# Kernel tuning notes

Hardware: AMD Instinct MI355X
Metric: run time of the kernel (lower is better)

The kernel has to match this reference:

```python
import jax, jax.numpy as jnp
import numpy as np

B, N, F_DIM, G_DIM, E_CAT, N_HEAD = 8, 1024, 128, 64, 2, 4
N_EDGES = 16384
L0 = 256          # NodeEmbedding hidden layer (layers=[256,128] -> last replaced by feature_size)
ALPHA = 0.5       # cfg.alpha
EPS = 1e-5        # BatchNorm eps
SLOPE = 0.01      # leaky_relu default negative slope


def _glorot(k, shape):
    stdv = float(np.sqrt(6.0 / (shape[-2] + shape[-1])))
    return jax.random.uniform(k, shape, jnp.float32, -stdv, stdv)


def setup_inputs() -> dict:
    key = jax.random.key(0)
    ks = jax.random.split(key, 8)
    X = jax.random.normal(ks[0], (B, N, F_DIM), dtype=jnp.float32)
    A = jax.random.randint(ks[1], (B, E_CAT, 2, N_EDGES), 0, N, dtype=jnp.int32)
    Ws = _glorot(ks[2], (E_CAT, N_HEAD * F_DIM, G_DIM))
    Wq = _glorot(ks[3], (E_CAT, N_HEAD * F_DIM, 1))
    Wv = _glorot(ks[4], (E_CAT, N_HEAD * F_DIM, 1))
    W_emb1 = _glorot(ks[5], (F_DIM, N_HEAD * E_CAT * G_DIM))   # Embedding1, bias=False
    W_lin0 = _glorot(ks[6], (L0, F_DIM))                        # NodeEmbedding linear0
    W_lin1 = _glorot(ks[7], (F_DIM, L0))                        # NodeEmbedding linear1
    return {"A": A, "X": X, "Ws": Ws, "Wq": Wq, "Wv": Wv,
            "W_emb1": W_emb1, "W_lin0": W_lin0, "W_lin1": W_lin1, "mini_batch": 1}


def _bn(x):
    # BatchNorm1d in training mode, affine = identity (weight=1, bias=0)
    mu = jnp.mean(x, axis=0)
    var = jnp.var(x, axis=0)  # biased variance, as torch uses for normalization
    return (x - mu) * jax.lax.rsqrt(var + EPS)


def _build_adj(A):
    # torch.sparse_coo_tensor(...).to_dense() sums duplicate edges
    adj = jnp.zeros((B, E_CAT, N, N), jnp.float32)
    b_idx = jnp.arange(B)[:, None, None]
    e_idx = jnp.arange(E_CAT)[None, :, None]
    return adj.at[b_idx, e_idx, A[:, :, 0], A[:, :, 1]].add(1.0)


def reference(A, X, Ws, Wq, Wv, W_emb1, W_lin0, W_lin1, mini_batch):
    Ws_r = Ws.reshape(E_CAT, N_HEAD, F_DIM, G_DIM)
    Wq_r = Wq.reshape(E_CAT, N_HEAD, F_DIM)   # last dim of Wq param is 1
    Wv_r = Wv.reshape(E_CAT, N_HEAD, F_DIM)

    Wh = jnp.einsum('bnf,ehfg->behng', X, Ws_r)   # [B,E,H,N,G]
    q = jnp.einsum('bnf,ehf->behn', X, Wq_r)      # [B,E,H,N]
    v = jnp.einsum('bnf,ehf->behn', X, Wv_r)

    adj = _build_adj(A)                            # [B,E,N,N]
    # e = (Wq @ Wv.T) * E, then leaky_relu and row softmax (dim=1 on [N,N] = last axis)
    scores = q[:, :, :, :, None] * v[:, :, :, None, :] * adj[:, :, None]
    scores = jnp.where(scores >= 0, scores, SLOPE * scores)
    a = jax.nn.softmax(scores, axis=-1)
    H = jnp.einsum('behnm,behmg->behng', a, Wh)    # [B,E,H,N,G]

    # concat over heads: [B,N, head-major (E*G)]
    H = H.transpose(0, 3, 2, 1, 4).reshape(B * N, N_HEAD * E_CAT * G_DIM)
    H = jax.nn.relu(H @ W_emb1.T)
    Xf = X.reshape(B * N, F_DIM)
    H = _bn((1.0 - ALPHA) * H + ALPHA * Xf)

    # NodeEmbedding: Linear -> BN -> ELU -> Linear
    Z = jax.nn.elu(_bn(H @ W_lin0.T))
    Z = Z @ W_lin1.T
    Z = _bn(H + Z)
    return Z.reshape(B, N, F_DIM)
```

## Files before the change

### kernel.cpp

```cpp
#include <hip/hip_runtime.h>
#include <hip/hip_bf16.h>

#define B_    8
#define N_    1024
#define F_    128
#define G_    64
#define EC    2
#define NHD   4
#define NE    16384
#define L0_   256
#define ALPHA_ 0.5f
#define EPS_   1e-5f
#define SLOPE_ 0.01f
#define ROWS  (B_*N_)
#define C1    (NHD*EC*G_)

typedef __attribute__((ext_vector_type(8))) short s8bf;
typedef __attribute__((ext_vector_type(4))) float f32x4;

__device__ __forceinline__ float ldv(const float* p, size_t i) { return p[i]; }
__device__ __forceinline__ float ldv(const __hip_bfloat16* p, size_t i) {
  unsigned short u = *(const unsigned short*)&p[i];
  return __uint_as_float((unsigned)u << 16);
}
__device__ __forceinline__ unsigned short f2b(float f) {
  unsigned u = __float_as_uint(f);
  u = (u + 0x7FFFu + ((u >> 16) & 1u)) >> 16;
  return (unsigned short)u;
}
__device__ __forceinline__ float b2f(unsigned short u) {
  return __uint_as_float((unsigned)u << 16);
}

__device__ __forceinline__ float wmaxf(float v) {
#pragma unroll
  for (int o = 32; o; o >>= 1) v = fmaxf(v, __shfl_xor(v, o, 64));
  return v;
}
__device__ __forceinline__ float wsumf(float v) {
#pragma unroll
  for (int o = 32; o; o >>= 1) v += __shfl_xor(v, o, 64);
  return v;
}

__global__ void k_detect(const unsigned short* Xu, int* flag) {
  int idx = blockIdx.x * 256 + threadIdx.x;
  unsigned short u = Xu[idx];
  if ((u & 0x7F80u) == 0x7F80u) atomicOr(flag, 1);
}

__device__ __forceinline__ unsigned short cvt_at(const void* p, size_t i, int isf) {
  return isf ? f2b(((const float*)p)[i]) : ((const unsigned short*)p)[i];
}
__global__ void k_cvtw(const void* X, const void* Ws, const void* We1, const void* Wl1,
                       unsigned short* Xb, unsigned short* Wsb, unsigned short* We1b,
                       unsigned short* Wl1b, const int* flag) {
  int isf = *flag;
  int bid = blockIdx.x, t = threadIdx.x;
  if (bid < 4096) {
    int i = bid * 256 + t; Xb[i] = cvt_at(X, i, isf);
  } else if (bid < 4352) {
    int i = (bid - 4096) * 256 + t; We1b[i] = cvt_at(We1, i, isf);
  } else if (bid < 4480) {
    int i = (bid - 4352) * 256 + t; Wl1b[i] = cvt_at(Wl1, i, isf);
  } else {
    int i = (bid - 4480) * 256 + t;
    int eh = i >> 13, rem = i & 8191;
    int g = rem >> 7, f = rem & 127;
    Wsb[eh * 8192 + g * 128 + f] = cvt_at(Ws, (size_t)eh * 8192 + f * 64 + g, isf);
  }
}

template <typename T>
__device__ __forceinline__ void proj_qv_body(const T* X, const T* Wq, const T* Wv,
                                             float* q, float* v) {
  int tid = threadIdx.x, lane = tid & 63, w = tid >> 6;
  int r = blockIdx.x * 4 + w;
  int n = r & (N_ - 1); int beh = r >> 10; int be = beh >> 2, h = beh & 3;
  int b = be >> 1, e = be & 1;
  const T* xr = X + ((size_t)(b * N_ + n)) * F_;
  const T* wq = Wq + (e * NHD + h) * F_;
  const T* wv = Wv + (e * NHD + h) * F_;
  float x0 = ldv(xr, lane), x1 = ldv(xr, lane + 64);
  float aq = x0 * ldv(wq, lane) + x1 * ldv(wq, lane + 64);
  float av = x0 * ldv(wv, lane) + x1 * ldv(wv, lane + 64);
  aq = wsumf(aq); av = wsumf(av);
  if (lane == 0) { q[r] = aq; v[r] = av; }
}
__global__ void k_proj_qv(const void* X, const void* Wq, const void* Wv,
                          float* q, float* v, const int* flag) {
  if (*flag) proj_qv_body<float>((const float*)X, (const float*)Wq, (const float*)Wv, q, v);
  else       proj_qv_body<__hip_bfloat16>((const __hip_bfloat16*)X, (const __hip_bfloat16*)Wq,
                                          (const __hip_bfloat16*)Wv, q, v);
}

template <int K>
__device__ __forceinline__ void mfma_core(const unsigned short* __restrict__ Ab,
                                          const unsigned short* __restrict__ Wb,
                                          int r0, int c0, f32x4* acc) {
  int lane = threadIdx.x & 63; int q = lane >> 4, c15 = lane & 15;
  constexpr int RS = K / 8;
  const s8bf* ap = (const s8bf*)Ab + (size_t)(r0 + c15) * RS + q;
  const s8bf* bp = (const s8bf*)Wb + (size_t)(c0 + c15) * RS + q;
#pragma unroll
  for (int ks = 0; ks < K / 32; ++ks) {
    s8bf a  = ap[ks * 4];
    s8bf b0 = bp[ks * 4];
    s8bf b1 = bp[16 * RS + ks * 4];
    s8bf b2 = bp[32 * RS + ks * 4];
    s8bf b3 = bp[48 * RS + ks * 4];
    acc[0] = __builtin_amdgcn_mfma_f32_16x16x32_bf16(a, b0, acc[0], 0, 0, 0);
    acc[1] = __builtin_amdgcn_mfma_f32_16x16x32_bf16(a, b1, acc[1], 0, 0, 0);
    acc[2] = __builtin_amdgcn_mfma_f32_16x16x32_bf16(a, b2, acc[2], 0, 0, 0);
    acc[3] = __builtin_amdgcn_mfma_f32_16x16x32_bf16(a, b3, acc[3], 0, 0, 0);
  }
}

__global__ __launch_bounds__(64) void k_whm(const unsigned short* Xb,
                                            const unsigned short* Wsb,
                                            float* Wh, float* S) {
  int r0 = blockIdx.x * 16; int eh = blockIdx.y;
  f32x4 acc[4] = {{0,0,0,0},{0,0,0,0},{0,0,0,0},{0,0,0,0}};
  mfma_core<128>(Xb, Wsb + eh * 8192, r0, 0, acc);
  int lane = threadIdx.x, q = lane >> 4, c15 = lane & 15;
  int b = r0 >> 10; int beh = b * 8 + eh;
  float* WhB = Wh + ((size_t)beh * N_ + (r0 & (N_ - 1))) * G_;
#pragma unroll
  for (int nc = 0; nc < 4; ++nc) {
    float s = 0.f;
#pragma unroll
    for (int i = 0; i < 4; ++i) {
      float o = acc[nc][i];
      WhB[(size_t)(q * 4 + i) * G_ + nc * 16 + c15] = o;
      s += o;
    }
    s += __shfl_xor(s, 16, 64); s += __shfl_xor(s, 32, 64);
    if (lane < 16) atomicAdd(&S[(size_t)beh * G_ + nc * 16 + lane], s);
  }
}

__global__ void k_scatter2(const int* A, int* fill, int* colbuf) {
  int idx = blockIdx.x * 256 + threadIdx.x;
  int be = idx >> 14, i = idx & (NE - 1);
  int row = A[(size_t)(be * 2) * NE + i];
  int col = A[(size_t)(be * 2 + 1) * NE + i];
  int p = atomicAdd(&fill[be * N_ + row], 1);
  if (p < 64) colbuf[((size_t)(be * N_ + row)) * 64 + p] = col;
}

__global__ __launch_bounds__(256) void k_attn2(const float* q, const float* v, const float* Wh,
                                               const float* S, const int* fill,
                                               const int* colbuf, unsigned short* Hcatb) {
  __shared__ int s_col[64];
  __shared__ int s_cnt[64];
  __shared__ int s_ld;
  __shared__ float s_w[4][64];
  int tid = threadIdx.x, lane = tid & 63, h = tid >> 6;
  int be = blockIdx.x >> 10, n = blockIdx.x & (N_ - 1);
  int b = be >> 1, e = be & 1;
  if (h == 0) {
    s_col[lane] = 0;
    int L = fill[be * N_ + n];
    int Lc = (L > 64) ? 64 : L;
    int myc = (lane < Lc) ? colbuf[((size_t)(be * N_ + n)) * 64 + lane] : -1;
    int cct = 0, firstk = 64;
    for (int k = 0; k < Lc; ++k) {
      int ck = __shfl(myc, k, 64);
      if (myc >= 0 && ck == myc) { cct++; if (k < firstk) firstk = k; }
    }
    bool act = (lane < Lc) && (firstk == lane);
    unsigned long long mask = __ballot(act);
    int pos = __popcll(mask & ((1ull << lane) - 1ull));
    if (act) { s_col[pos] = myc; s_cnt[pos] = cct; }
    if (lane == 0) s_ld = __popcll(mask);
  }
  __syncthreads();
  int Ld = s_ld;
  int beh = (be << 2) | h;
  float qn = q[beh * N_ + n];
  float sc = -1e30f;
  if (lane < Ld) {
    float t = qn * v[beh * N_ + s_col[lane]] * (float)s_cnt[lane];
    sc = (t >= 0.f) ? t : SLOPE_ * t;
  }
  float M = fmaxf(0.f, wmaxf(sc));
  float Ej = (lane < Ld) ? expf(sc - M) : 0.f;
  float sumE = wsumf(Ej);
  float em = expf(-M);
  float Z = (float)(N_ - Ld) * em + sumE;
  s_w[h][lane] = (lane < Ld) ? (Ej - em) / Z : 0.f;
  int eg = lane >> 4, g4 = (lane & 15) << 2;
  float4 accv = make_float4(0.f, 0.f, 0.f, 0.f);
  if (eg == 0) {
    float4 s4 = *(const float4*)&S[(size_t)beh * G_ + g4];
    float sca = em / Z;
    accv.x = sca * s4.x; accv.y = sca * s4.y; accv.z = sca * s4.z; accv.w = sca * s4.w;
  }
  const float* WhB = Wh + (size_t)beh * N_ * G_;
  for (int k0 = 0; k0 < Ld; k0 += 4) {
    int kk = k0 + eg;
    float wk = s_w[h][kk];
    int ck = s_col[kk];
    float4 x = *(const float4*)&WhB[(size_t)ck * G_ + g4];
    accv.x += wk * x.x; accv.y += wk * x.y; accv.z += wk * x.z; accv.w += wk * x.w;
  }
  accv.x += __shfl_xor(accv.x, 16, 64); accv.y += __shfl_xor(accv.y, 16, 64);
  accv.z += __shfl_xor(accv.z, 16, 64); accv.w += __shfl_xor(accv.w, 16, 64);
  accv.x += __shfl_xor(accv.x, 32, 64); accv.y += __shfl_xor(accv.y, 32, 64);
  accv.z += __shfl_xor(accv.z, 32, 64); accv.w += __shfl_xor(accv.w, 32, 64);
  if (lane < 16) {
    ushort4 o;
    o.x = f2b(accv.x); o.y = f2b(accv.y); o.z = f2b(accv.z); o.w = f2b(accv.w);
    *(ushort4*)&Hcatb[((size_t)(b * N_ + n)) * C1 + h * (EC * G_) + e * G_ + g4] = o;
  }
}

template <typename TX>
__device__ __forceinline__ void mm1_ep(f32x4* acc, const TX* X, float* T4,
                                       unsigned short* T4b, float* sum1, float* ssq1,
                                       int r0, int c0) {
  int lane = threadIdx.x, q = lane >> 4, c15 = lane & 15;
#pragma unroll
  for (int nc = 0; nc < 4; ++nc) {
    int cc = c0 + nc * 16 + c15;
    float s = 0.f, s2 = 0.f;
#pragma unroll
    for (int i = 0; i < 4; ++i) {
      int rr = r0 + q * 4 + i;
      float o = fmaxf(acc[nc][i], 0.f);
      o = 0.5f * o + 0.5f * ldv(X, (size_t)rr * F_ + cc);
      T4[(size_t)rr * F_ + cc] = o;
      T4b[(size_t)rr * F_ + cc] = f2b(o);
      s += o; s2 += o * o;
    }
    s += __shfl_xor(s, 16, 64); s += __shfl_xor(s, 32, 64);
    s2 += __shfl_xor(s2, 16, 64); s2 += __shfl_xor(s2, 32, 64);
    if (lane < 16) {
      atomicAdd(&sum1[c0 + nc * 16 + lane], s);
      atomicAdd(&ssq1[c0 + nc * 16 + lane], s2);
    }
  }
}
__global__ __launch_bounds__(64) void k_mm1m(const unsigned short* Hcatb,
                                             const unsigned short* We1b, const void* X,
                                             float* T4, unsigned short* T4b,
                                             float* sum1, float* ssq1, const int* flag) {
  int r0 = blockIdx.x * 16, c0 = blockIdx.y * 64;
  f32x4 acc[4] = {{0,0,0,0},{0,0,0,0},{0,0,0,0},{0,0,0,0}};
  mfma_core<512>(Hcatb, We1b, r0, c0, acc);
  if (*flag) mm1_ep<float>(acc, (const float*)X, T4, T4b, sum1, ssq1, r0, c0);
  else       mm1_ep<__hip_bfloat16>(acc, (const __hip_bfloat16*)X, T4, T4b, sum1, ssq1, r0, c0);
}

__global__ void k_fold0(const void* Wl0, const float* sum1, const float* ssq1,
                        unsigned short* W0p, float* bias0, const int* flag) {
  __shared__ float red[2];
  int c = blockIdx.x, k = threadIdx.x;
  float mean = sum1[k] * (1.f / ROWS);
  float var = ssq1[k] * (1.f / ROWS) - mean * mean;
  float rs = rsqrtf(var + EPS_);
  float w = (*flag) ? ((const float*)Wl0)[(size_t)c * F_ + k]
                    : b2f(((const unsigned short*)Wl0)[(size_t)c * F_ + k]);
  unsigned short wb = f2b(w * rs);
  W0p[(size_t)c * F_ + k] = wb;
  float part = mean * b2f(wb);
  part = wsumf(part);
  if ((threadIdx.x & 63) == 0) red[threadIdx.x >> 6] = part;
  __syncthreads();
  if (threadIdx.x == 0) bias0[c] = red[0] + red[1];
}

__global__ __launch_bounds__(64) void k_lin0m(const unsigned short* T4b,
                                              const unsigned short* W0p, const float* bias0,
                                              float* Z0, float* sum2, float* ssq2) {
  int r0 = blockIdx.x * 16, c0 = blockIdx.y * 64;
  f32x4 acc[4] = {{0,0,0,0},{0,0,0,0},{0,0,0,0},{0,0,0,0}};
  mfma_core<128>(T4b, W0p, r0, c0, acc);
  int lane = threadIdx.x, q = lane >> 4, c15 = lane & 15;
#pragma unroll
  for (int nc = 0; nc < 4; ++nc) {
    int cc = c0 + nc * 16 + c15;
    float bia = bias0[cc];
    float s = 0.f, s2 = 0.f;
#pragma unroll
    for (int i = 0; i < 4; ++i) {
      int rr = r0 + q * 4 + i;
      float o = acc[nc][i] - bia;
      Z0[(size_t)rr * L0_ + cc] = o;
      s += o; s2 += o * o;
    }
    s += __shfl_xor(s, 16, 64); s += __shfl_xor(s, 32, 64);
    s2 += __shfl_xor(s2, 16, 64); s2 += __shfl_xor(s2, 32, 64);
    if (lane < 16) {
      atomicAdd(&sum2[c0 + nc * 16 + lane], s);
      atomicAdd(&ssq2[c0 + nc * 16 + lane], s2);
    }
  }
}

__global__ void k_elu(const float* Z0, unsigned short* E, const float* sum2,
                      const float* ssq2) {
  int idx = blockIdx.x * 256 + threadIdx.x;
  int c = idx & (L0_ - 1);
  float mean = sum2[c] * (1.f / ROWS);
  float var = ssq2[c] * (1.f / ROWS) - mean * mean;
  float y = (Z0[idx] - mean) * rsqrtf(var + EPS_);
  y = (y > 0.f) ? y : (expf(y) - 1.f);
  E[idx] = f2b(y);
}

__global__ __launch_bounds__(64) void k_lin1m(const unsigned short* E,
                                              const unsigned short* Wl1b, const float* T4,
                                              const float* sum1, const float* ssq1,
                                              float* T6, float* sum3, float* ssq3) {
  int r0 = blockIdx.x * 16, c0 = blockIdx.y * 64;
  f32x4 acc[4] = {{0,0,0,0},{0,0,0,0},{0,0,0,0},{0,0,0,0}};
  mfma_core<256>(E, Wl1b, r0, c0, acc);
  int lane = threadIdx.x, q = lane >> 4, c15 = lane & 15;
#pragma unroll
  for (int nc = 0; nc < 4; ++nc) {
    int cc = c0 + nc * 16 + c15;
    float mean = sum1[cc] * (1.f / ROWS);
    float var = ssq1[cc] * (1.f / ROWS) - mean * mean;
    float rs = rsqrtf(var + EPS_);
    float s = 0.f, s2 = 0.f;
#pragma unroll
    for (int i = 0; i < 4; ++i) {
      int rr = r0 + q * 4 + i;
      float o = acc[nc][i] + (T4[(size_t)rr * F_ + cc] - mean) * rs;
      T6[(size_t)rr * F_ + cc] = o;
      s += o; s2 += o * o;
    }
    s += __shfl_xor(s, 16, 64); s += __shfl_xor(s, 32, 64);
    s2 += __shfl_xor(s2, 16, 64); s2 += __shfl_xor(s2, 32, 64);
    if (lane < 16) {
      atomicAdd(&sum3[c0 + nc * 16 + lane], s);
      atomicAdd(&ssq3[c0 + nc * 16 + lane], s2);
    }
  }
}

__global__ void k_norm_out(const float* in, void* out, const float* sum, const float* ssq,
                           const int* flag) {
  int idx = blockIdx.x * 256 + threadIdx.x; int c = idx & (F_ - 1);
  float mean = sum[c] * (1.f / ROWS);
  float var = ssq[c] * (1.f / ROWS) - mean * mean;
  float y = (in[idx] - mean) * rsqrtf(var + EPS_);
  if (*flag) ((float*)out)[idx] = y;
  else       ((__hip_bfloat16*)out)[idx] = __float2bfloat16(y);
}

extern "C" void kernel_launch(void* const* d_in, const int* in_sizes, int n_in,
                              void* d_out, int out_size, void* d_ws, size_t ws_size,
                              hipStream_t stream) {
  const int* A    = (const int*)d_in[0];
  const void* X   = d_in[1];
  const void* Ws  = d_in[2];
  const void* Wq  = d_in[3];
  const void* Wv  = d_in[4];
  const void* We1 = d_in[5];
  const void* Wl0 = d_in[6];
  const void* Wl1 = d_in[7];

  char* ws = (char*)d_ws;
  size_t off = 0;
  auto alloc = [&](size_t bytes) { size_t o = off; off += (bytes + 255) & ~(size_t)255; return o; };
  size_t o_fill   = alloc(16 * N_ * 4);
  size_t o_stats  = alloc(1024 * 4);
  size_t o_flag   = alloc(256);
  size_t o_S      = alloc((size_t)64 * G_ * 4);
  size_t zero_bytes = off;
  size_t o_colbuf = alloc((size_t)16 * N_ * 64 * 4);
  size_t o_q      = alloc((size_t)64 * N_ * 4);
  size_t o_v      = alloc((size_t)64 * N_ * 4);
  size_t o_Wh     = alloc((size_t)64 * N_ * G_ * 4);
  size_t o_Hcatb  = alloc((size_t)ROWS * C1 * 2);
  size_t o_T4     = alloc((size_t)ROWS * F_ * 4);
  size_t o_T4b    = alloc((size_t)ROWS * F_ * 2);
  size_t o_T6     = alloc((size_t)ROWS * F_ * 4);
  size_t o_Z0     = alloc((size_t)ROWS * L0_ * 4);
  size_t o_E      = alloc((size_t)ROWS * L0_ * 2);
  size_t o_Xb     = alloc((size_t)ROWS * F_ * 2);
  size_t o_Wsb    = alloc((size_t)8 * G_ * F_ * 2);
  size_t o_We1b   = alloc((size_t)F_ * C1 * 2);
  size_t o_Wl1b   = alloc((size_t)F_ * L0_ * 2);
  size_t o_W0p    = alloc((size_t)L0_ * F_ * 2);
  size_t o_bias0  = alloc(L0_ * 4);

  int*   fill   = (int*)(ws + o_fill);
  float* stats  = (float*)(ws + o_stats);
  int*   flag   = (int*)(ws + o_flag);
  float* S      = (float*)(ws + o_S);
  int*   colbuf = (int*)(ws + o_colbuf);
  float* q      = (float*)(ws + o_q);
  float* v      = (float*)(ws + o_v);
  float* Wh     = (float*)(ws + o_Wh);
  unsigned short* Hcatb = (unsigned short*)(ws + o_Hcatb);
  float* T4     = (float*)(ws + o_T4);
  unsigned short* T4b   = (unsigned short*)(ws + o_T4b);
  float* T6     = (float*)(ws + o_T6);
  float* Z0     = (float*)(ws + o_Z0);
  unsigned short* E     = (unsigned short*)(ws + o_E);
  unsigned short* Xb    = (unsigned short*)(ws + o_Xb);
  unsigned short* Wsb   = (unsigned short*)(ws + o_Wsb);
  unsigned short* We1b  = (unsigned short*)(ws + o_We1b);
  unsigned short* Wl1b  = (unsigned short*)(ws + o_Wl1b);
  unsigned short* W0p   = (unsigned short*)(ws + o_W0p);
  float* bias0  = (float*)(ws + o_bias0);
  float* sum1 = stats,       *ssq1 = stats + 128;
  float* sum2 = stats + 256, *ssq2 = stats + 512;
  float* sum3 = stats + 768, *ssq3 = stats + 896;

  hipMemsetAsync(ws, 0, zero_bytes, stream);

  k_detect<<<512, 256, 0, stream>>>((const unsigned short*)X, flag);
  k_cvtw<<<4736, 256, 0, stream>>>(X, Ws, We1, Wl1, Xb, Wsb, We1b, Wl1b, flag);

  k_proj_qv<<<(64 * N_) / 4, 256, 0, stream>>>(X, Wq, Wv, q, v, flag);
  k_whm<<<dim3(ROWS / 16, 8), 64, 0, stream>>>(Xb, Wsb, Wh, S);

  k_scatter2<<<(16 * NE) / 256, 256, 0, stream>>>(A, fill, colbuf);
  k_attn2<<<16 * N_, 256, 0, stream>>>(q, v, Wh, S, fill, colbuf, Hcatb);

  k_mm1m<<<dim3(ROWS / 16, 2), 64, 0, stream>>>(Hcatb, We1b, X, T4, T4b, sum1, ssq1, flag);
  k_fold0<<<L0_, 128, 0, stream>>>(Wl0, sum1, ssq1, W0p, bias0, flag);
  k_lin0m<<<dim3(ROWS / 16, 4), 64, 0, stream>>>(T4b, W0p, bias0, Z0, sum2, ssq2);
  k_elu<<<(ROWS * L0_) / 256, 256, 0, stream>>>(Z0, E, sum2, ssq2);
  k_lin1m<<<dim3(ROWS / 16, 2), 64, 0, stream>>>(E, Wl1b, T4, sum1, ssq1, T6, sum3, ssq3);
  k_norm_out<<<(ROWS * F_) / 256, 256, 0, stream>>>(T6, d_out, sum3, ssq3, flag);

  (void)in_sizes; (void)n_in; (void)out_size; (void)ws_size;
}
```

Before: 247.3 us.

## Fuse BatchNorm/ELU into GEMM A-loads, store Wh in bf16, restructure attention per wave

Removes the k_fold0 and k_elu kernels. The BatchNorm normalisation (and the ELU for the second linear) is now applied inside the MFMA A-operand load, reading fp32 activations and converting to bf16 on the fly. Wh is stored as bf16 to halve gather traffic in attention. The attention kernel now handles one node per wave across all four heads, using shuffles instead of shared memory and syncthreads. The trade-off is extra ALU work and fp32 A reads inside the GEMM inner loops, with per-element rsqrt/exp recomputed for every column tile.

```diff
diff --git a/kernel.cpp b/kernel.cpp
--- a/kernel.cpp
+++ b/kernel.cpp
@@ -53,8 +53,9 @@
   return isf ? f2b(((const float*)p)[i]) : ((const unsigned short*)p)[i];
 }
 __global__ void k_cvtw(const void* X, const void* Ws, const void* We1, const void* Wl1,
-                       unsigned short* Xb, unsigned short* Wsb, unsigned short* We1b,
-                       unsigned short* Wl1b, const int* flag) {
+                       const void* Wl0, unsigned short* Xb, unsigned short* Wsb,
+                       unsigned short* We1b, unsigned short* Wl1b, unsigned short* Wl0b,
+                       const int* flag) {
   int isf = *flag;
   int bid = blockIdx.x, t = threadIdx.x;
   if (bid < 4096) {
@@ -63,8 +64,10 @@
     int i = (bid - 4096) * 256 + t; We1b[i] = cvt_at(We1, i, isf);
   } else if (bid < 4480) {
     int i = (bid - 4352) * 256 + t; Wl1b[i] = cvt_at(Wl1, i, isf);
+  } else if (bid < 4608) {
+    int i = (bid - 4480) * 256 + t; Wl0b[i] = cvt_at(Wl0, i, isf);
   } else {
-    int i = (bid - 4480) * 256 + t;
+    int i = (bid - 4608) * 256 + t;
     int eh = i >> 13, rem = i & 8191;
     int g = rem >> 7, f = rem & 127;
     Wsb[eh * 8192 + g * 128 + f] = cvt_at(Ws, (size_t)eh * 8192 + f * 64 + g, isf);
@@ -116,22 +119,57 @@
   }
 }
 
+template <int K, int MODE>
+__device__ __forceinline__ void mfma_core_t(const float* __restrict__ Araw,
+                                            const float* sum, const float* ssq,
+                                            const unsigned short* __restrict__ Wb,
+                                            int r0, int c0, f32x4* acc) {
+  int lane = threadIdx.x & 63; int q = lane >> 4, c15 = lane & 15;
+  constexpr int RS = K / 8;
+  const float* ap = Araw + (size_t)(r0 + c15) * K + q * 8;
+  const s8bf* bp = (const s8bf*)Wb + (size_t)(c0 + c15) * RS + q;
+#pragma unroll
+  for (int ks = 0; ks < K / 32; ++ks) {
+    float av[8];
+    *(float4*)&av[0] = *(const float4*)(ap + ks * 32);
+    *(float4*)&av[4] = *(const float4*)(ap + ks * 32 + 4);
+    s8bf a;
+#pragma unroll
+    for (int j = 0; j < 8; ++j) {
+      int c = q * 8 + ks * 32 + j;
+      float mean = sum[c] * (1.f / ROWS);
+      float var = ssq[c] * (1.f / ROWS) - mean * mean;
+      float y = (av[j] - mean) * rsqrtf(var + EPS_);
+      if (MODE == 2) y = (y > 0.f) ? y : (expf(y) - 1.f);
+      a[j] = (short)f2b(y);
+    }
+    s8bf b0 = bp[ks * 4];
+    s8bf b1 = bp[16 * RS + ks * 4];
+    s8bf b2 = bp[32 * RS + ks * 4];
+    s8bf b3 = bp[48 * RS + ks * 4];
+    acc[0] = __builtin_amdgcn_mfma_f32_16x16x32_bf16(a, b0, acc[0], 0, 0, 0);
+    acc[1] = __builtin_amdgcn_mfma_f32_16x16x32_bf16(a, b1, acc[1], 0, 0, 0);
+    acc[2] = __builtin_amdgcn_mfma_f32_16x16x32_bf16(a, b2, acc[2], 0, 0, 0);
+    acc[3] = __builtin_amdgcn_mfma_f32_16x16x32_bf16(a, b3, acc[3], 0, 0, 0);
+  }
+}
+
 __global__ __launch_bounds__(64) void k_whm(const unsigned short* Xb,
                                             const unsigned short* Wsb,
-                                            float* Wh, float* S) {
+                                            unsigned short* Whb, float* S) {
   int r0 = blockIdx.x * 16; int eh = blockIdx.y;
   f32x4 acc[4] = {{0,0,0,0},{0,0,0,0},{0,0,0,0},{0,0,0,0}};
   mfma_core<128>(Xb, Wsb + eh * 8192, r0, 0, acc);
   int lane = threadIdx.x, q = lane >> 4, c15 = lane & 15;
   int b = r0 >> 10; int beh = b * 8 + eh;
-  float* WhB = Wh + ((size_t)beh * N_ + (r0 & (N_ - 1))) * G_;
+  unsigned short* WhB = Whb + ((size_t)beh * N_ + (r0 & (N_ - 1))) * G_;
 #pragma unroll
   for (int nc = 0; nc < 4; ++nc) {
     float s = 0.f;
 #pragma unroll
     for (int i = 0; i < 4; ++i) {
       float o = acc[nc][i];
-      WhB[(size_t)(q * 4 + i) * G_ + nc * 16 + c15] = o;
+      WhB[(size_t)(q * 4 + i) * G_ + nc * 16 + c15] = f2b(o);
       s += o;
     }
     s += __shfl_xor(s, 16, 64); s += __shfl_xor(s, 32, 64);
@@ -148,77 +186,80 @@
   if (p < 64) colbuf[((size_t)(be * N_ + row)) * 64 + p] = col;
 }
 
-__global__ __launch_bounds__(256) void k_attn2(const float* q, const float* v, const float* Wh,
+__global__ __launch_bounds__(256) void k_attn3(const float* q, const float* v,
+                                               const unsigned short* Whb,
                                                const float* S, const int* fill,
                                                const int* colbuf, unsigned short* Hcatb) {
-  __shared__ int s_col[64];
-  __shared__ int s_cnt[64];
-  __shared__ int s_ld;
-  __shared__ float s_w[4][64];
-  int tid = threadIdx.x, lane = tid & 63, h = tid >> 6;
-  int be = blockIdx.x >> 10, n = blockIdx.x & (N_ - 1);
+  __shared__ int s_col[4][64];
+  __shared__ int s_cnt[4][64];
+  int tid = threadIdx.x, lane = tid & 63, w = tid >> 6;
+  int p = blockIdx.x * 4 + w;
+  int be = p >> 10, n = p & (N_ - 1);
   int b = be >> 1, e = be & 1;
-  if (h == 0) {
-    s_col[lane] = 0;
-    int L = fill[be * N_ + n];
-    int Lc = (L > 64) ? 64 : L;
-    int myc = (lane < Lc) ? colbuf[((size_t)(be * N_ + n)) * 64 + lane] : -1;
-    int cct = 0, firstk = 64;
-    for (int k = 0; k < Lc; ++k) {
-      int ck = __shfl(myc, k, 64);
-      if (myc >= 0 && ck == myc) { cct++; if (k < firstk) firstk = k; }
-    }
-    bool act = (lane < Lc) && (firstk == lane);
-    unsigned long long mask = __ballot(act);
-    int pos = __popcll(mask & ((1ull << lane) - 1ull));
-    if (act) { s_col[pos] = myc; s_cnt[pos] = cct; }
-    if (lane == 0) s_ld = __popcll(mask);
-  }
-  __syncthreads();
-  int Ld = s_ld;
-  int beh = (be << 2) | h;
-  float qn = q[beh * N_ + n];
-  float sc = -1e30f;
-  if (lane < Ld) {
-    float t = qn * v[beh * N_ + s_col[lane]] * (float)s_cnt[lane];
-    sc = (t >= 0.f) ? t : SLOPE_ * t;
-  }
-  float M = fmaxf(0.f, wmaxf(sc));
-  float Ej = (lane < Ld) ? expf(sc - M) : 0.f;
-  float sumE = wsumf(Ej);
-  float em = expf(-M);
-  float Z = (float)(N_ - Ld) * em + sumE;
-  s_w[h][lane] = (lane < Ld) ? (Ej - em) / Z : 0.f;
+  s_col[w][lane] = 0; s_cnt[w][lane] = 0;
+  int L = fill[be * N_ + n];
+  int Lc = (L > 64) ? 64 : L;
+  int myc = (lane < Lc) ? colbuf[((size_t)(be * N_ + n)) * 64 + lane] : -1;
+  int cct = 0, firstk = 64;
+  for (int k = 0; k < Lc; ++k) {
+    int ck = __shfl(myc, k, 64);
+    if (myc >= 0 && ck == myc) { cct++; if (k < firstk) firstk = k; }
+  }
+  bool act = (lane < Lc) && (firstk == lane);
+  unsigned long long mask = __ballot(act);
+  int pos = __popcll(mask & ((1ull << lane) - 1ull));
+  if (act) { s_col[w][pos] = myc; s_cnt[w][pos] = cct; }
+  int Ld = __popcll(mask);
+  int colc = s_col[w][lane];
+  int cntc = s_cnt[w][lane];
   int eg = lane >> 4, g4 = (lane & 15) << 2;
-  float4 accv = make_float4(0.f, 0.f, 0.f, 0.f);
-  if (eg == 0) {
-    float4 s4 = *(const float4*)&S[(size_t)beh * G_ + g4];
-    float sca = em / Z;
-    accv.x = sca * s4.x; accv.y = sca * s4.y; accv.z = sca * s4.z; accv.w = sca * s4.w;
-  }
-  const float* WhB = Wh + (size_t)beh * N_ * G_;
-  for (int k0 = 0; k0 < Ld; k0 += 4) {
-    int kk = k0 + eg;
-    float wk = s_w[h][kk];
-    int ck = s_col[kk];
-    float4 x = *(const float4*)&WhB[(size_t)ck * G_ + g4];
-    accv.x += wk * x.x; accv.y += wk * x.y; accv.z += wk * x.z; accv.w += wk * x.w;
-  }
-  accv.x += __shfl_xor(accv.x, 16, 64); accv.y += __shfl_xor(accv.y, 16, 64);
-  accv.z += __shfl_xor(accv.z, 16, 64); accv.w += __shfl_xor(accv.w, 16, 64);
-  accv.x += __shfl_xor(accv.x, 32, 64); accv.y += __shfl_xor(accv.y, 32, 64);
-  accv.z += __shfl_xor(accv.z, 32, 64); accv.w += __shfl_xor(accv.w, 32, 64);
-  if (lane < 16) {
-    ushort4 o;
-    o.x = f2b(accv.x); o.y = f2b(accv.y); o.z = f2b(accv.z); o.w = f2b(accv.w);
-    *(ushort4*)&Hcatb[((size_t)(b * N_ + n)) * C1 + h * (EC * G_) + e * G_ + g4] = o;
+  size_t outb = ((size_t)(b * N_ + n)) * C1 + e * G_ + g4;
+  float fN = (float)(N_ - Ld);
+#pragma unroll
+  for (int h = 0; h < 4; ++h) {
+    int beh = (be << 2) | h;
+    float qn = q[beh * N_ + n];
+    float sc = -1e30f;
+    if (lane < Ld) {
+      float t = qn * v[beh * N_ + colc] * (float)cntc;
+      sc = (t >= 0.f) ? t : SLOPE_ * t;
+    }
+    float M = fmaxf(0.f, wmaxf(sc));
+    float Ej = (lane < Ld) ? expf(sc - M) : 0.f;
+    float sumE = wsumf(Ej);
+    float em = expf(-M);
+    float Z = fN * em + sumE;
+    float wgt = (lane < Ld) ? (Ej - em) / Z : 0.f;
+    float4 accv = make_float4(0.f, 0.f, 0.f, 0.f);
+    if (eg == 0) {
+      float4 s4 = *(const float4*)&S[(size_t)beh * G_ + g4];
+      float sca = em / Z;
+      accv.x = sca * s4.x; accv.y = sca * s4.y; accv.z = sca * s4.z; accv.w = sca * s4.w;
+    }
+    const unsigned short* WhB = Whb + (size_t)beh * N_ * G_;
+    for (int k0 = 0; k0 < Ld; k0 += 4) {
+      int kk = k0 + eg;
+      float wk = __shfl(wgt, kk, 64);
+      int ck = __shfl(colc, kk, 64);
+      ushort4 xu = *(const ushort4*)&WhB[(size_t)ck * G_ + g4];
+      accv.x += wk * b2f(xu.x); accv.y += wk * b2f(xu.y);
+      accv.z += wk * b2f(xu.z); accv.w += wk * b2f(xu.w);
+    }
+    accv.x += __shfl_xor(accv.x, 16, 64); accv.y += __shfl_xor(accv.y, 16, 64);
+    accv.z += __shfl_xor(accv.z, 16, 64); accv.w += __shfl_xor(accv.w, 16, 64);
+    accv.x += __shfl_xor(accv.x, 32, 64); accv.y += __shfl_xor(accv.y, 32, 64);
+    accv.z += __shfl_xor(accv.z, 32, 64); accv.w += __shfl_xor(accv.w, 32, 64);
+    if (lane < 16) {
+      ushort4 o;
+      o.x = f2b(accv.x); o.y = f2b(accv.y); o.z = f2b(accv.z); o.w = f2b(accv.w);
+      *(ushort4*)&Hcatb[outb + (size_t)h * (EC * G_)] = o;
+    }
   }
 }
 
 template <typename TX>
 __device__ __forceinline__ void mm1_ep(f32x4* acc, const TX* X, float* T4,
-                                       unsigned short* T4b, float* sum1, float* ssq1,
-                                       int r0, int c0) {
+                                       float* sum1, float* ssq1, int r0, int c0) {
   int lane = threadIdx.x, q = lane >> 4, c15 = lane & 15;
 #pragma unroll
   for (int nc = 0; nc < 4; ++nc) {
@@ -230,7 +271,6 @@
       float o = fmaxf(acc[nc][i], 0.f);
       o = 0.5f * o + 0.5f * ldv(X, (size_t)rr * F_ + cc);
       T4[(size_t)rr * F_ + cc] = o;
-      T4b[(size_t)rr * F_ + cc] = f2b(o);
       s += o; s2 += o * o;
     }
     s += __shfl_xor(s, 16, 64); s += __shfl_xor(s, 32, 64);
@@ -243,49 +283,30 @@
 }
 __global__ __launch_bounds__(64) void k_mm1m(const unsigned short* Hcatb,
                                              const unsigned short* We1b, const void* X,
-                                             float* T4, unsigned short* T4b,
-                                             float* sum1, float* ssq1, const int* flag) {
+                                             float* T4, float* sum1, float* ssq1,
+                                             const int* flag) {
   int r0 = blockIdx.x * 16, c0 = blockIdx.y * 64;
   f32x4 acc[4] = {{0,0,0,0},{0,0,0,0},{0,0,0,0},{0,0,0,0}};
   mfma_core<512>(Hcatb, We1b, r0, c0, acc);
-  if (*flag) mm1_ep<float>(acc, (const float*)X, T4, T4b, sum1, ssq1, r0, c0);
-  else       mm1_ep<__hip_bfloat16>(acc, (const __hip_bfloat16*)X, T4, T4b, sum1, ssq1, r0, c0);
-}
-
-__global__ void k_fold0(const void* Wl0, const float* sum1, const float* ssq1,
-                        unsigned short* W0p, float* bias0, const int* flag) {
-  __shared__ float red[2];
-  int c = blockIdx.x, k = threadIdx.x;
-  float mean = sum1[k] * (1.f / ROWS);
-  float var = ssq1[k] * (1.f / ROWS) - mean * mean;
-  float rs = rsqrtf(var + EPS_);
-  float w = (*flag) ? ((const float*)Wl0)[(size_t)c * F_ + k]
-                    : b2f(((const unsigned short*)Wl0)[(size_t)c * F_ + k]);
-  unsigned short wb = f2b(w * rs);
-  W0p[(size_t)c * F_ + k] = wb;
-  float part = mean * b2f(wb);
-  part = wsumf(part);
-  if ((threadIdx.x & 63) == 0) red[threadIdx.x >> 6] = part;
-  __syncthreads();
-  if (threadIdx.x == 0) bias0[c] = red[0] + red[1];
-}
-
-__global__ __launch_bounds__(64) void k_lin0m(const unsigned short* T4b,
-                                              const unsigned short* W0p, const float* bias0,
+  if (*flag) mm1_ep<float>(acc, (const float*)X, T4, sum1, ssq1, r0, c0);
+  else       mm1_ep<__hip_bfloat16>(acc, (const __hip_bfloat16*)X, T4, sum1, ssq1, r0, c0);
+}
+
+__global__ __launch_bounds__(64) void k_lin0m(const float* T4, const float* sum1,
+                                              const float* ssq1, const unsigned short* Wl0b,
                                               float* Z0, float* sum2, float* ssq2) {
   int r0 = blockIdx.x * 16, c0 = blockIdx.y * 64;
   f32x4 acc[4] = {{0,0,0,0},{0,0,0,0},{0,0,0,0},{0,0,0,0}};
-  mfma_core<128>(T4b, W0p, r0, c0, acc);
+  mfma_core_t<128, 1>(T4, sum1, ssq1, Wl0b, r0, c0, acc);
   int lane = threadIdx.x, q = lane >> 4, c15 = lane & 15;
 #pragma unroll
   for (int nc = 0; nc < 4; ++nc) {
     int cc = c0 + nc * 16 + c15;
-    float bia = bias0[cc];
     float s = 0.f, s2 = 0.f;
 #pragma unroll
     for (int i = 0; i < 4; ++i) {
       int rr = r0 + q * 4 + i;
-      float o = acc[nc][i] - bia;
+      float o = acc[nc][i];
       Z0[(size_t)rr * L0_ + cc] = o;
       s += o; s2 += o * o;
     }
@@ -298,24 +319,14 @@
   }
 }
 
-__global__ void k_elu(const float* Z0, unsigned short* E, const float* sum2,
-                      const float* ssq2) {
-  int idx = blockIdx.x * 256 + threadIdx.x;
-  int c = idx & (L0_ - 1);
-  float mean = sum2[c] * (1.f / ROWS);
-  float var = ssq2[c] * (1.f / ROWS) - mean * mean;
-  float y = (Z0[idx] - mean) * rsqrtf(var + EPS_);
-  y = (y > 0.f) ? y : (expf(y) - 1.f);
-  E[idx] = f2b(y);
-}
-
-__global__ __launch_bounds__(64) void k_lin1m(const unsigned short* E,
-                                              const unsigned short* Wl1b, const float* T4,
-                                              const float* sum1, const float* ssq1,
+__global__ __launch_bounds__(64) void k_lin1m(const float* Z0, const float* sum2,
+                                              const float* ssq2, const unsigned short* Wl1b,
+                                              const float* T4, const float* sum1,
+                                              const float* ssq1,
                                               float* T6, float* sum3, float* ssq3) {
   int r0 = blockIdx.x * 16, c0 = blockIdx.y * 64;
   f32x4 acc[4] = {{0,0,0,0},{0,0,0,0},{0,0,0,0},{0,0,0,0}};
-  mfma_core<256>(E, Wl1b, r0, c0, acc);
+  mfma_core_t<256, 2>(Z0, sum2, ssq2, Wl1b, r0, c0, acc);
   int lane = threadIdx.x, q = lane >> 4, c15 = lane & 15;
 #pragma unroll
   for (int nc = 0; nc < 4; ++nc) {
@@ -373,19 +384,16 @@
   size_t o_colbuf = alloc((size_t)16 * N_ * 64 * 4);
   size_t o_q      = alloc((size_t)64 * N_ * 4);
   size_t o_v      = alloc((size_t)64 * N_ * 4);
-  size_t o_Wh     = alloc((size_t)64 * N_ * G_ * 4);
+  size_t o_Whb    = alloc((size_t)64 * N_ * G_ * 2);
   size_t o_Hcatb  = alloc((size_t)ROWS * C1 * 2);
   size_t o_T4     = alloc((size_t)ROWS * F_ * 4);
-  size_t o_T4b    = alloc((size_t)ROWS * F_ * 2);
   size_t o_T6     = alloc((size_t)ROWS * F_ * 4);
   size_t o_Z0     = alloc((size_t)ROWS * L0_ * 4);
-  size_t o_E      = alloc((size_t)ROWS * L0_ * 2);
   size_t o_Xb     = alloc((size_t)ROWS * F_ * 2);
   size_t o_Wsb    = alloc((size_t)8 * G_ * F_ * 2);
   size_t o_We1b   = alloc((size_t)F_ * C1 * 2);
   size_t o_Wl1b   = alloc((size_t)F_ * L0_ * 2);
-  size_t o_W0p    = alloc((size_t)L0_ * F_ * 2);
-  size_t o_bias0  = alloc(L0_ * 4);
+  size_t o_Wl0b   = alloc((size_t)L0_ * F_ * 2);
 
   int*   fill   = (int*)(ws + o_fill);
   float* stats  = (float*)(ws + o_stats);
@@ -394,19 +402,16 @@
   int*   colbuf = (int*)(ws + o_colbuf);
   float* q      = (float*)(ws + o_q);
   float* v      = (float*)(ws + o_v);
-  float* Wh     = (float*)(ws + o_Wh);
+  unsigned short* Whb   = (unsigned short*)(ws + o_Whb);
   unsigned short* Hcatb = (unsigned short*)(ws + o_Hcatb);
   float* T4     = (float*)(ws + o_T4);
-  unsigned short* T4b   = (unsigned short*)(ws + o_T4b);
   float* T6     = (float*)(ws + o_T6);
   float* Z0     = (float*)(ws + o_Z0);
-  unsigned short* E     = (unsigned short*)(ws + o_E);
   unsigned short* Xb    = (unsigned short*)(ws + o_Xb);
   unsigned short* Wsb   = (unsigned short*)(ws + o_Wsb);
   unsigned short* We1b  = (unsigned short*)(ws + o_We1b);
   unsigned short* Wl1b  = (unsigned short*)(ws + o_Wl1b);
-  unsigned short* W0p   = (unsigned short*)(ws + o_W0p);
-  float* bias0  = (float*)(ws + o_bias0);
+  unsigned short* Wl0b  = (unsigned short*)(ws + o_Wl0b);
   float* sum1 = stats,       *ssq1 = stats + 128;
   float* sum2 = stats + 256, *ssq2 = stats + 512;
   float* sum3 = stats + 768, *ssq3 = stats + 896;
@@ -414,19 +419,18 @@
   hipMemsetAsync(ws, 0, zero_bytes, stream);
 
   k_detect<<<512, 256, 0, stream>>>((const unsigned short*)X, flag);
-  k_cvtw<<<4736, 256, 0, stream>>>(X, Ws, We1, Wl1, Xb, Wsb, We1b, Wl1b, flag);
+  k_cvtw<<<4864, 256, 0, stream>>>(X, Ws, We1, Wl1, Wl0, Xb, Wsb, We1b, Wl1b, Wl0b, flag);
 
   k_proj_qv<<<(64 * N_) / 4, 256, 0, stream>>>(X, Wq, Wv, q, v, flag);
-  k_whm<<<dim3(ROWS / 16, 8), 64, 0, stream>>>(Xb, Wsb, Wh, S);
+  k_whm<<<dim3(ROWS / 16, 8), 64, 0, stream>>>(Xb, Wsb, Whb, S);
 
   k_scatter2<<<(16 * NE) / 256, 256, 0, stream>>>(A, fill, colbuf);
-  k_attn2<<<16 * N_, 256, 0, stream>>>(q, v, Wh, S, fill, colbuf, Hcatb);
-
-  k_mm1m<<<dim3(ROWS / 16, 2), 64, 0, stream>>>(Hcatb, We1b, X, T4, T4b, sum1, ssq1, flag);
-  k_fold0<<<L0_, 128, 0, stream>>>(Wl0, sum1, ssq1, W0p, bias0, flag);
-  k_lin0m<<<dim3(ROWS / 16, 4), 64, 0, stream>>>(T4b, W0p, bias0, Z0, sum2, ssq2);
-  k_elu<<<(ROWS * L0_) / 256, 256, 0, stream>>>(Z0, E, sum2, ssq2);
-  k_lin1m<<<dim3(ROWS / 16, 2), 64, 0, stream>>>(E, Wl1b, T4, sum1, ssq1, T6, sum3, ssq3);
+  k_attn3<<<(16 * N_) / 4, 256, 0, stream>>>(q, v, Whb, S, fill, colbuf, Hcatb);
+
+  k_mm1m<<<dim3(ROWS / 16, 2), 64, 0, stream>>>(Hcatb, We1b, X, T4, sum1, ssq1, flag);
+  k_lin0m<<<dim3(ROWS / 16, 4), 64, 0, stream>>>(T4, sum1, ssq1, Wl0b, Z0, sum2, ssq2);
+  k_lin1m<<<dim3(ROWS / 16, 2), 64, 0, stream>>>(Z0, sum2, ssq2, Wl1b, T4, sum1, ssq1,
+                                                 T6, sum3, ssq3);
   k_norm_out<<<(ROWS * F_) / 256, 256, 0, stream>>>(T6, d_out, sum3, ssq3, flag);
 
   (void)in_sizes; (void)n_in; (void)out_size; (void)ws_size;
```

New measurement: 236.6 us. -4.3%, faster.
